# Performance work log

Hardware: AMD Instinct MI355X
Metric: run time of the kernel (lower is better)

The kernel has to match this reference:

```python
import jax, jax.numpy as jnp
import numpy as np

NUM_EXPERTS = 8
K = 2
N_EMBD = 1024
HIDDEN = 4 * N_EMBD
BATCH = 2
SEQ = 1024
LB_SCALE = 0.01
NOISY_STD = 1.0
INIT_S = 0.02


def setup_inputs() -> dict:
    key = jax.random.key(0)
    ks = jax.random.split(key, 8)
    D, H, E = N_EMBD, HIDDEN, NUM_EXPERTS
    return {
        "x": jax.random.normal(ks[0], (BATCH, SEQ, D), jnp.float32),
        "noise": jax.random.normal(ks[1], (BATCH, SEQ, E), jnp.float32),  # torch.randn_like(logits)
        "gate_w": jax.random.normal(ks[2], (E, D), jnp.float32) * INIT_S,
        "noise_weight": jnp.zeros((E,), jnp.float32),  # initialized to zeros in the module
        "w1": jax.random.normal(ks[3], (E, H, D), jnp.float32) * INIT_S,
        "b1": jnp.zeros((E, H), jnp.float32),
        "w2": jax.random.normal(ks[4], (E, H, D), jnp.float32) * INIT_S,
        "b2": jnp.zeros((E, H), jnp.float32),
        "wp": jax.random.normal(ks[5], (E, D, H), jnp.float32) * INIT_S,
        "bp": jnp.zeros((E, D), jnp.float32),
    }


def reference(x, noise, gate_w, noise_weight, w1, b1, w2, b2, wp, bp):
    B, S, D = x.shape
    E = gate_w.shape[0]

    # ---- TopKGateParallel ----
    logits = jnp.einsum('bsd,ed->bse', x, gate_w)           # [B,S,E]
    gate_weights = jax.nn.softmax(logits, axis=-1)
    gw_mean = gate_weights.reshape(-1, E).mean(axis=0)       # [E]
    load_balance_loss = jnp.mean((gw_mean - 1.0 / E) ** 2) * LB_SCALE  # mse vs uniform

    logits_noisy = logits + (noise * NOISY_STD) * noise_weight
    top_v, top_i = jax.lax.top_k(logits_noisy, K)            # [B,S,K]
    # scatter top-k logits into a -inf sea, then softmax -> zeros at non-topk slots
    topk_mask = jnp.sum(jax.nn.one_hot(top_i, E, dtype=jnp.float32), axis=-2) > 0  # [B,S,E]
    sparse_logits = jnp.where(topk_mask, logits_noisy, -jnp.inf)
    top_k_gated_weights = jax.nn.softmax(sparse_logits, axis=-1)  # [B,S,E]

    # ---- expert compute + weighted combine (world_size=1: all experts local) ----
    x_flat = x.reshape(B * S, D)                              # [T,D]
    w_flat = top_k_gated_weights.reshape(B * S, E)            # [T,E]
    y = jnp.zeros_like(x_flat)
    for e in range(E):  # fixed small set of experts
        h = x_flat @ w1[e].T + b1[e]                          # [T,H]
        g = x_flat @ w2[e].T + b2[e]                          # [T,H]
        out_e = (h * jax.nn.silu(g)) @ wp[e].T + bp[e]        # [T,D]
        y = y + w_flat[:, e:e + 1] * out_e
    y = y.reshape(B, S, D)
    return y, load_balance_loss
```

## Files before the change

kernel.cpp:

```cpp
#include <hip/hip_runtime.h>

#define TOK 2048
#define DIM 1024
#define HID 4096
#define NE 8
#define KSPLIT 8
#define TMAX 24

typedef unsigned short u16;
typedef __attribute__((ext_vector_type(8))) short s16x8;
typedef __attribute__((ext_vector_type(4))) float f32x4;

__device__ __forceinline__ u16 f2b(float f) {
  unsigned u = __builtin_bit_cast(unsigned, f);
  unsigned r = (u + 0x7fffu + ((u >> 16) & 1u)) >> 16;
  return (u16)r;
}

__device__ __forceinline__ void gld_lds16(const void* g, void* l) {
  __builtin_amdgcn_global_load_lds((const __attribute__((address_space(1))) void*)g,
                                   (__attribute__((address_space(3))) void*)l, 16, 0, 0);
}

__global__ __launch_bounds__(256) void k_gate(const float* __restrict__ x,
    const float* __restrict__ noise, const float* __restrict__ gw,
    const float* __restrict__ nw,
    int* __restrict__ tok_e, float* __restrict__ tok_w,
    int* __restrict__ bhist, float* __restrict__ bgw, u16* __restrict__ x16) {
  const int wid = threadIdx.x >> 6, lane = threadIdx.x & 63;
  const int t = blockIdx.x * 4 + wid;
  const float* xr = x + (size_t)t * DIM + lane * 16;
  float acc[NE];
#pragma unroll
  for (int e = 0; e < NE; ++e) acc[e] = 0.f;
  u16 xb[16];
#pragma unroll
  for (int j = 0; j < 4; ++j) {
    float4 xv = *(const float4*)(xr + j * 4);
    xb[j * 4 + 0] = f2b(xv.x); xb[j * 4 + 1] = f2b(xv.y);
    xb[j * 4 + 2] = f2b(xv.z); xb[j * 4 + 3] = f2b(xv.w);
#pragma unroll
    for (int e = 0; e < NE; ++e) {
      float4 gv = *(const float4*)(gw + e * DIM + lane * 16 + j * 4);
      acc[e] += xv.x * gv.x + xv.y * gv.y + xv.z * gv.z + xv.w * gv.w;
    }
  }
  *(s16x8*)(x16 + (size_t)t * DIM + lane * 16) = *(const s16x8*)xb;
  *(s16x8*)(x16 + (size_t)t * DIM + lane * 16 + 8) = *(const s16x8*)(xb + 8);
#pragma unroll
  for (int e = 0; e < NE; ++e) {
#pragma unroll
    for (int off = 32; off >= 1; off >>= 1) acc[e] += __shfl_xor(acc[e], off);
  }
  float m = acc[0];
#pragma unroll
  for (int e = 1; e < NE; ++e) m = fmaxf(m, acc[e]);
  float p[NE]; float s = 0.f;
#pragma unroll
  for (int e = 0; e < NE; ++e) { p[e] = expf(acc[e] - m); s += p[e]; }
  float inv = 1.f / s;
  float v[NE];
#pragma unroll
  for (int e = 0; e < NE; ++e) v[e] = acc[e] + noise[t * NE + e] * nw[e];
  float v0 = -3.4e38f, v1 = -3.4e38f; int i0 = 0, i1 = 0;
#pragma unroll
  for (int e = 0; e < NE; ++e) {
    float ve = v[e];
    if (ve > v0) { v1 = v0; i1 = i0; v0 = ve; i0 = e; }
    else if (ve > v1) { v1 = ve; i1 = e; }
  }
  float e1 = expf(v1 - v0);
  float den = 1.f + e1;
  float w0 = 1.f / den, w1v = e1 / den;

  __shared__ float pl[4][NE];
  __shared__ int el[4][2];
  if (lane == 0) {
#pragma unroll
    for (int e = 0; e < NE; ++e) pl[wid][e] = p[e] * inv;
    el[wid][0] = i0; el[wid][1] = i1;
    tok_e[t * 2] = i0; tok_e[t * 2 + 1] = i1;
    tok_w[t * 2] = w0; tok_w[t * 2 + 1] = w1v;
  }
  __syncthreads();
  if (threadIdx.x < NE) {
    const int e = threadIdx.x;
    float ps = pl[0][e] + pl[1][e] + pl[2][e] + pl[3][e];
    int h = 0;
#pragma unroll
    for (int j = 0; j < 4; ++j) {
      h += (el[j][0] == e);
      h += (el[j][1] == e);
    }
    bgw[blockIdx.x * NE + e] = ps;
    bhist[blockIdx.x * NE + e] = h;
  }
}

__global__ __launch_bounds__(512) void k_scan(const int* __restrict__ bhist,
    const float* __restrict__ bgw, int* __restrict__ blk_off, int* __restrict__ prefix,
    int* __restrict__ counts, int* __restrict__ tile_tab, float* __restrict__ loss_out) {
  const int i = threadIdx.x, lane = i & 63, wv = i >> 6;
  __shared__ int wsum[8];
  __shared__ float wfs[8];
  __shared__ int etot[8];
  __shared__ float fsum[8];
  for (int e = 0; e < NE; ++e) {
    int v = bhist[i * NE + e];
    int sc = v;
#pragma unroll
    for (int off = 1; off < 64; off <<= 1) {
      int u = __shfl_up(sc, off);
      if (lane >= off) sc += u;
    }
    float f = bgw[i * NE + e];
#pragma unroll
    for (int off = 32; off >= 1; off >>= 1) f += __shfl_xor(f, off);
    if (lane == 63) wsum[wv] = sc;
    if (lane == 0) wfs[wv] = f;
    __syncthreads();
    int base = 0;
    for (int w2 = 0; w2 < wv; ++w2) base += wsum[w2];
    blk_off[i * NE + e] = base + sc - v;
    if (i == 0) {
      float tf = 0.f;
      for (int w2 = 0; w2 < 8; ++w2) tf += wfs[w2];
      fsum[e] = tf;
    }
    if (i == 511) etot[e] = base + sc;
    __syncthreads();
  }
  if (i == 0) {
    int sacc = 0;
    float l = 0.f;
    int tt = 0;
#pragma unroll
    for (int e = 0; e < NE; ++e) { prefix[e] = sacc; counts[e] = etot[e]; sacc += etot[e]; }
    for (int e = 0; e < NE; ++e) {
      const int nmt = (etot[e] + 255) >> 8;
      for (int m2 = 0; m2 < nmt; ++m2) tile_tab[tt++] = (e << 16) | m2;
    }
    for (; tt < TMAX; ++tt) tile_tab[tt] = -1;
#pragma unroll
    for (int e = 0; e < NE; ++e) {
      float d = fsum[e] * (1.f / TOK) - 0.125f;
      l += d * d;
    }
    *loss_out = l * (0.01f / NE);
  }
}

__global__ __launch_bounds__(256) void k_build(const int* __restrict__ tok_e,
    const float* __restrict__ tok_w, const int* __restrict__ prefix,
    const int* __restrict__ blk_off, int* __restrict__ ent, float* __restrict__ entw,
    int* __restrict__ inv) {
  const int t = blockIdx.x * 256 + threadIdx.x;
  const int g = t >> 2;
  const int base = (t & 3) * 2;
  int ee[8];
#pragma unroll
  for (int j = 0; j < 8; ++j) ee[j] = tok_e[g * 8 + j];
#pragma unroll
  for (int s = 0; s < 2; ++s) {
    const int e = ee[base + s];
    int rank = 0;
#pragma unroll
    for (int j = 0; j < 8; ++j) rank += (j < base + s) && (ee[j] == e);
    const int idx = prefix[e] + blk_off[g * NE + e] + rank;
    ent[idx] = t * 2 + s;
    entw[idx] = tok_w[t * 2 + s];
    inv[t * 2 + s] = idx;
  }
}

__global__ __launch_bounds__(512) void k_gemm1f(const u16* __restrict__ x16,
    const float* __restrict__ w1, const float* __restrict__ w2,
    const float* __restrict__ b1, const float* __restrict__ b2,
    const int* __restrict__ ent, const int* __restrict__ counts,
    const int* __restrict__ prefix, const int* __restrict__ tile_tab,
    u16* __restrict__ act) {
  const int tt = tile_tab[blockIdx.y];
  if (tt < 0) return;
  const int e = tt >> 16, mt = tt & 0xffff, nt = blockIdx.x;
  const int cnt = counts[e];
  const int pfx = prefix[e];
  const int tid = threadIdx.x, w = tid >> 6, l = tid & 63;

  __shared__ u16 smem[2][16384];

  const int r0 = tid >> 2;
  const int c = (tid & 3) ^ ((tid >> 3) & 3);
  int g0 = mt * 256 + r0;       if (g0 >= cnt) g0 = cnt - 1;
  int g1 = mt * 256 + 128 + r0; if (g1 >= cnt) g1 = cnt - 1;
  const u16* sa0 = x16 + (size_t)(ent[pfx + g0] >> 1) * DIM + c * 8;
  const u16* sa1 = x16 + (size_t)(ent[pfx + g1] >> 1) * DIM + c * 8;
  const float* pB1 = w1 + ((size_t)e * HID + nt * 128 + r0) * DIM + c * 8;
  const float* pB2 = w2 + ((size_t)e * HID + nt * 128 + r0) * DIM + c * 8;
  const int oA0 = tid * 8, oA1 = 4096 + tid * 8;
  const int oB1 = 8192 + tid * 8, oB2 = 12288 + tid * 8;

  const int wr = w >> 1, wc = w & 1;
  const int xs = ((l >> 4) ^ ((l >> 1) & 3)) * 8;
  const int ra = (wr * 64 + (l & 15)) * 32 + xs;
  const int rb = (wc * 64 + (l & 15)) * 32 + xs;

  f32x4 acc1[4][4], acc2[4][4];
#pragma unroll
  for (int m = 0; m < 4; ++m)
#pragma unroll
    for (int n = 0; n < 4; ++n) {
      acc1[m][n] = (f32x4){0.f, 0.f, 0.f, 0.f};
      acc2[m][n] = (f32x4){0.f, 0.f, 0.f, 0.f};
    }

  f32x4 a0_, a1_, a2_, a3_;
  f32x4 b0_, b1_, b2_, b3_;

  auto LOADB = [&](f32x4& r0_, f32x4& r1_, f32x4& r2_, f32x4& r3_, int k0) {
    r0_ = *(const f32x4*)(pB1 + k0);
    r1_ = *(const f32x4*)(pB1 + k0 + 4);
    r2_ = *(const f32x4*)(pB2 + k0);
    r3_ = *(const f32x4*)(pB2 + k0 + 4);
  };
  auto STAGEA = [&](int buf, int k0) {
    gld_lds16(sa0 + k0, &smem[buf][oA0]);
    gld_lds16(sa1 + k0, &smem[buf][oA1]);
  };
  auto WRITEB = [&](int buf, const f32x4& r0_, const f32x4& r1_,
                    const f32x4& r2_, const f32x4& r3_) {
    u16 u[16];
    u[0] = f2b(r0_[0]); u[1] = f2b(r0_[1]); u[2] = f2b(r0_[2]); u[3] = f2b(r0_[3]);
    u[4] = f2b(r1_[0]); u[5] = f2b(r1_[1]); u[6] = f2b(r1_[2]); u[7] = f2b(r1_[3]);
    u[8] = f2b(r2_[0]); u[9] = f2b(r2_[1]); u[10] = f2b(r2_[2]); u[11] = f2b(r2_[3]);
    u[12] = f2b(r3_[0]); u[13] = f2b(r3_[1]); u[14] = f2b(r3_[2]); u[15] = f2b(r3_[3]);
    *(s16x8*)&smem[buf][oB1] = *(const s16x8*)u;
    *(s16x8*)&smem[buf][oB2] = *(const s16x8*)(u + 8);
  };
  auto MSTEP = [&](int cur) {
    const u16* S = &smem[cur][0];
    s16x8 af[4];
#pragma unroll
    for (int m = 0; m < 4; ++m) af[m] = *(const s16x8*)(S + ra + m * 512);
    __builtin_amdgcn_s_setprio(1);
#pragma unroll
    for (int n = 0; n < 4; ++n) {
      s16x8 bf1 = *(const s16x8*)(S + 8192 + rb + n * 512);
      s16x8 bf2 = *(const s16x8*)(S + 12288 + rb + n * 512);
#pragma unroll
      for (int m = 0; m < 4; ++m) {
        acc1[m][n] = __builtin_amdgcn_mfma_f32_16x16x32_bf16(af[m], bf1, acc1[m][n], 0, 0, 0);
        acc2[m][n] = __builtin_amdgcn_mfma_f32_16x16x32_bf16(af[m], bf2, acc2[m][n], 0, 0, 0);
      }
    }
    __builtin_amdgcn_s_setprio(0);
  };

  const int NT = DIM / 32;
  LOADB(a0_, a1_, a2_, a3_, 0);
  STAGEA(0, 0);
  LOADB(b0_, b1_, b2_, b3_, 32);
  asm volatile("s_waitcnt vmcnt(4)" ::: "memory");
  __builtin_amdgcn_sched_barrier(0);
  WRITEB(0, a0_, a1_, a2_, a3_);
  STAGEA(1, 32);
  asm volatile("s_waitcnt lgkmcnt(0)" ::: "memory");
  __builtin_amdgcn_sched_barrier(0);
  __builtin_amdgcn_s_barrier();

  for (int kt = 0; kt < NT; kt += 2) {
    if (kt + 2 < NT) LOADB(a0_, a1_, a2_, a3_, (kt + 2) * 32);
    MSTEP(0);
    __builtin_amdgcn_s_barrier();
    if (kt + 2 < NT) asm volatile("s_waitcnt vmcnt(4)" ::: "memory");
    else             asm volatile("s_waitcnt vmcnt(0)" ::: "memory");
    __builtin_amdgcn_sched_barrier(0);
    WRITEB(1, b0_, b1_, b2_, b3_);
    if (kt + 2 < NT) STAGEA(0, (kt + 2) * 32);
    asm volatile("s_waitcnt lgkmcnt(0)" ::: "memory");
    __builtin_amdgcn_sched_barrier(0);
    __builtin_amdgcn_s_barrier();
    if (kt + 3 < NT) LOADB(b0_, b1_, b2_, b3_, (kt + 3) * 32);
    MSTEP(1);
    if (kt + 2 < NT) {
      __builtin_amdgcn_s_barrier();
      if (kt + 3 < NT) asm volatile("s_waitcnt vmcnt(4)" ::: "memory");
      else             asm volatile("s_waitcnt vmcnt(0)" ::: "memory");
      __builtin_amdgcn_sched_barrier(0);
      WRITEB(0, a0_, a1_, a2_, a3_);
      if (kt + 3 < NT) STAGEA(1, (kt + 3) * 32);
      asm volatile("s_waitcnt lgkmcnt(0)" ::: "memory");
      __builtin_amdgcn_sched_barrier(0);
      __builtin_amdgcn_s_barrier();
    }
  }

#pragma unroll
  for (int n = 0; n < 4; ++n) {
    const int col = nt * 128 + wc * 64 + n * 16 + (l & 15);
    const float bb1 = b1[(size_t)e * HID + col];
    const float bb2 = b2[(size_t)e * HID + col];
#pragma unroll
    for (int m = 0; m < 4; ++m) {
#pragma unroll
      for (int r = 0; r < 4; ++r) {
        const int row = mt * 256 + wr * 64 + m * 16 + (l >> 4) * 4 + r;
        if (row < cnt) {
          float h = acc1[m][n][r] + bb1;
          float g = acc2[m][n][r] + bb2;
          float a = h * g / (1.f + expf(-g));
          act[(size_t)(pfx + row) * HID + col] = f2b(a);
        }
      }
    }
  }
}

__global__ __launch_bounds__(512) void k_gemm2f(const u16* __restrict__ act,
    const float* __restrict__ wp, const float* __restrict__ bp,
    const float* __restrict__ entw, const int* __restrict__ counts,
    const int* __restrict__ prefix, const int* __restrict__ tile_tab,
    float* __restrict__ yp) {
  const int tt = tile_tab[blockIdx.y];
  if (tt < 0) return;
  const int e = tt >> 16, mt = tt & 0xffff;
  const int sk = blockIdx.z, nt = blockIdx.x;
  const int cnt = counts[e];
  const int pfx = prefix[e];
  const int tid = threadIdx.x, w = tid >> 6, l = tid & 63;

  __shared__ u16 smem[2][16384];

  const int r0 = tid >> 2;
  const int c = (tid & 3) ^ ((tid >> 3) & 3);
  int g0 = mt * 256 + r0;       if (g0 >= cnt) g0 = cnt - 1;
  int g1 = mt * 256 + 128 + r0; if (g1 >= cnt) g1 = cnt - 1;
  const int kbase = sk * (HID / KSPLIT);
  const u16* sa0 = act + (size_t)(pfx + g0) * HID + kbase + c * 8;
  const u16* sa1 = act + (size_t)(pfx + g1) * HID + kbase + c * 8;
  const float* pB0 = wp + ((size_t)e * DIM + nt * 256 + r0) * HID + kbase + c * 8;
  const float* pB1h = pB0 + (size_t)128 * HID;
  const int oA0 = tid * 8, oA1 = 4096 + tid * 8;
  const int oB0 = 8192 + tid * 8, oB1 = 12288 + tid * 8;

  const int wr = w >> 2, wc = w & 3;
  const int xs = ((l >> 4) ^ ((l >> 1) & 3)) * 8;
  const int ra = (wr * 128 + (l & 15)) * 32 + xs;
  const int rb = 8192 + (wc * 64 + (l & 15)) * 32 + xs;

  f32x4 acc[8][4];
#pragma unroll
  for (int m = 0; m < 8; ++m)
#pragma unroll
    for (int n = 0; n < 4; ++n) acc[m][n] = (f32x4){0.f, 0.f, 0.f, 0.f};

  f32x4 a0_, a1_, a2_, a3_;
  f32x4 b0_, b1_, b2_, b3_;

  auto LOADB = [&](f32x4& r0_, f32x4& r1_, f32x4& r2_, f32x4& r3_, int k0) {
    r0_ = *(const f32x4*)(pB0 + k0);
    r1_ = *(const f32x4*)(pB0 + k0 + 4);
    r2_ = *(const f32x4*)(pB1h + k0);
    r3_ = *(const f32x4*)(pB1h + k0 + 4);
  };
  auto STAGEA = [&](int buf, int k0) {
    gld_lds16(sa0 + k0, &smem[buf][oA0]);
    gld_lds16(sa1 + k0, &smem[buf][oA1]);
  };
  auto WRITEB = [&](int buf, const f32x4& r0_, const f32x4& r1_,
                    const f32x4& r2_, const f32x4& r3_) {
    u16 u[16];
    u[0] = f2b(r0_[0]); u[1] = f2b(r0_[1]); u[2] = f2b(r0_[2]); u[3] = f2b(r0_[3]);
    u[4] = f2b(r1_[0]); u[5] = f2b(r1_[1]); u[6] = f2b(r1_[2]); u[7] = f2b(r1_[3]);
    u[8] = f2b(r2_[0]); u[9] = f2b(r2_[1]); u[10] = f2b(r2_[2]); u[11] = f2b(r2_[3]);
    u[12] = f2b(r3_[0]); u[13] = f2b(r3_[1]); u[14] = f2b(r3_[2]); u[15] = f2b(r3_[3]);
    *(s16x8*)&smem[buf][oB0] = *(const s16x8*)u;
    *(s16x8*)&smem[buf][oB1] = *(const s16x8*)(u + 8);
  };
  auto MSTEP = [&](int cur) {
    const u16* S = &smem[cur][0];
    __builtin_amdgcn_s_setprio(1);
#pragma unroll
    for (int n = 0; n < 4; ++n) {
      s16x8 bf = *(const s16x8*)(S + rb + n * 512);
#pragma unroll
      for (int m = 0; m < 8; ++m) {
        s16x8 af = *(const s16x8*)(S + ra + m * 512);
        acc[m][n] = __builtin_amdgcn_mfma_f32_16x16x32_bf16(af, bf, acc[m][n], 0, 0, 0);
      }
    }
    __builtin_amdgcn_s_setprio(0);
  };

  const int NIT = HID / KSPLIT / 32;
  LOADB(a0_, a1_, a2_, a3_, 0);
  STAGEA(0, 0);
  LOADB(b0_, b1_, b2_, b3_, 32);
  asm volatile("s_waitcnt vmcnt(4)" ::: "memory");
  __builtin_amdgcn_sched_barrier(0);
  WRITEB(0, a0_, a1_, a2_, a3_);
  STAGEA(1, 32);
  asm volatile("s_waitcnt lgkmcnt(0)" ::: "memory");
  __builtin_amdgcn_sched_barrier(0);
  __builtin_amdgcn_s_barrier();

  for (int kt = 0; kt < NIT; kt += 2) {
    if (kt + 2 < NIT) LOADB(a0_, a1_, a2_, a3_, (kt + 2) * 32);
    MSTEP(0);
    __builtin_amdgcn_s_barrier();
    if (kt + 2 < NIT) asm volatile("s_waitcnt vmcnt(4)" ::: "memory");
    else              asm volatile("s_waitcnt vmcnt(0)" ::: "memory");
    __builtin_amdgcn_sched_barrier(0);
    WRITEB(1, b0_, b1_, b2_, b3_);
    if (kt + 2 < NIT) STAGEA(0, (kt + 2) * 32);
    asm volatile("s_waitcnt lgkmcnt(0)" ::: "memory");
    __builtin_amdgcn_sched_barrier(0);
    __builtin_amdgcn_s_barrier();
    if (kt + 3 < NIT) LOADB(b0_, b1_, b2_, b3_, (kt + 3) * 32);
    MSTEP(1);
    if (kt + 2 < NIT) {
      __builtin_amdgcn_s_barrier();
      if (kt + 3 < NIT) asm volatile("s_waitcnt vmcnt(4)" ::: "memory");
      else              asm volatile("s_waitcnt vmcnt(0)" ::: "memory");
      __builtin_amdgcn_sched_barrier(0);
      WRITEB(0, a0_, a1_, a2_, a3_);
      if (kt + 3 < NIT) STAGEA(1, (kt + 3) * 32);
      asm volatile("s_waitcnt lgkmcnt(0)" ::: "memory");
      __builtin_amdgcn_sched_barrier(0);
      __builtin_amdgcn_s_barrier();
    }
  }

#pragma unroll
  for (int n = 0; n < 4; ++n) {
    const int col = nt * 256 + wc * 64 + n * 16 + (l & 15);
    const float bpv = (sk == 0) ? bp[(size_t)e * DIM + col] : 0.f;
#pragma unroll
    for (int m = 0; m < 8; ++m) {
#pragma unroll
      for (int r = 0; r < 4; ++r) {
        const int row = mt * 256 + wr * 128 + m * 16 + (l >> 4) * 4 + r;
        if (row < cnt) {
          const int idx = pfx + row;
          yp[((size_t)sk * (TOK * 2) + idx) * DIM + col] = entw[idx] * (acc[m][n][r] + bpv);
        }
      }
    }
  }
}

__global__ __launch_bounds__(256) void k_final(const float* __restrict__ yp,
    const int* __restrict__ inv, float* __restrict__ out) {
  const int t = blockIdx.x;
  const int d = threadIdx.x * 4;
  const int i0 = inv[t * 2], i1 = inv[t * 2 + 1];
  float4 s = {0.f, 0.f, 0.f, 0.f};
#pragma unroll
  for (int sk = 0; sk < KSPLIT; ++sk) {
    float4 a = *(const float4*)(yp + ((size_t)sk * (TOK * 2) + i0) * DIM + d);
    float4 b = *(const float4*)(yp + ((size_t)sk * (TOK * 2) + i1) * DIM + d);
    s.x += a.x + b.x; s.y += a.y + b.y; s.z += a.z + b.z; s.w += a.w + b.w;
  }
  *(float4*)(out + (size_t)t * DIM + d) = s;
}

extern "C" void kernel_launch(void* const* d_in, const int* in_sizes, int n_in,
                              void* d_out, int out_size, void* d_ws, size_t ws_size,
                              hipStream_t stream) {
  const float* x      = (const float*)d_in[0];
  const float* noise  = (const float*)d_in[1];
  const float* gate_w = (const float*)d_in[2];
  const float* nw     = (const float*)d_in[3];
  const float* w1     = (const float*)d_in[4];
  const float* b1     = (const float*)d_in[5];
  const float* w2     = (const float*)d_in[6];
  const float* b2     = (const float*)d_in[7];
  const float* wp     = (const float*)d_in[8];
  const float* bp     = (const float*)d_in[9];
  float* out = (float*)d_out;
  char* ws = (char*)d_ws;

  const size_t SZ_X16 = (size_t)TOK * DIM * 2;
  const size_t SZ_ACT = (size_t)TOK * 2 * HID * 2;
  const size_t SZ_YP  = (size_t)KSPLIT * TOK * 2 * DIM * 4;

  u16* x16  = (u16*)ws;
  u16* act  = (u16*)(ws + SZ_X16);
  float* yp = (float*)(ws + SZ_X16 + SZ_ACT);
  char* meta = ws + SZ_X16 + SZ_ACT + SZ_YP;
  int*   tok_e    = (int*)(meta);
  float* tok_w    = (float*)(meta + 16384);
  int*   ent      = (int*)(meta + 32768);
  float* entw     = (float*)(meta + 49152);
  int*   bhist    = (int*)(meta + 65536);
  float* bgw      = (float*)(meta + 81920);
  int*   blk_off  = (int*)(meta + 98304);
  int*   inv      = (int*)(meta + 114688);
  int*   counts   = (int*)(meta + 131072);
  int*   prefix   = (int*)(meta + 131072 + 64);
  int*   tile_tab = (int*)(meta + 131072 + 128);

  k_gate<<<TOK / 4, 256, 0, stream>>>(x, noise, gate_w, nw, tok_e, tok_w, bhist, bgw, x16);
  k_scan<<<1, 512, 0, stream>>>(bhist, bgw, blk_off, prefix, counts, tile_tab,
                                out + (size_t)TOK * DIM);
  k_build<<<TOK / 256, 256, 0, stream>>>(tok_e, tok_w, prefix, blk_off, ent, entw, inv);
  k_gemm1f<<<dim3(HID / 128, TMAX), 512, 0, stream>>>(x16, w1, w2, b1, b2, ent,
                                                      counts, prefix, tile_tab, act);
  k_gemm2f<<<dim3(DIM / 256, TMAX, KSPLIT), 512, 0, stream>>>(act, wp, bp, entw,
                                                              counts, prefix, tile_tab, yp);
  k_final<<<TOK, 256, 0, stream>>>(yp, inv, out);
}
```

Baseline: 348.3 us.

## Double K-tile depth to 64 in both expert GEMMs and halve K-split

Both grouped GEMM kernels now stage a 64-wide K slice per pipeline step instead of 32. This doubles the LDS buffers to 64 KB each and re-derives the XOR swizzle for 8 chunks per row. Each step issues two MFMA sub-steps, which halves the number of barriers and waitcnt round trips per K. The second GEMM's split-K factor drops from 8 to 4, reducing partial-sum writes and the reduction traffic at the cost of fewer blocks. The trade-offs are higher register pressure (16 staged f32x4 vectors), larger LDS use that may cap occupancy, and less parallelism in the second GEMM.

```diff
diff --git a/kernel.cpp b/kernel.cpp
--- a/kernel.cpp
+++ b/kernel.cpp
@@ -4,7 +4,7 @@
 #define DIM 1024
 #define HID 4096
 #define NE 8
-#define KSPLIT 8
+#define KSPLIT 4
 #define TMAX 24
 
 typedef unsigned short u16;
@@ -186,23 +186,35 @@
   const int pfx = prefix[e];
   const int tid = threadIdx.x, w = tid >> 6, l = tid & 63;
 
-  __shared__ u16 smem[2][16384];
-
-  const int r0 = tid >> 2;
-  const int c = (tid & 3) ^ ((tid >> 3) & 3);
-  int g0 = mt * 256 + r0;       if (g0 >= cnt) g0 = cnt - 1;
-  int g1 = mt * 256 + 128 + r0; if (g1 >= cnt) g1 = cnt - 1;
-  const u16* sa0 = x16 + (size_t)(ent[pfx + g0] >> 1) * DIM + c * 8;
-  const u16* sa1 = x16 + (size_t)(ent[pfx + g1] >> 1) * DIM + c * 8;
-  const float* pB1 = w1 + ((size_t)e * HID + nt * 128 + r0) * DIM + c * 8;
-  const float* pB2 = w2 + ((size_t)e * HID + nt * 128 + r0) * DIM + c * 8;
-  const int oA0 = tid * 8, oA1 = 4096 + tid * 8;
-  const int oB1 = 8192 + tid * 8, oB2 = 12288 + tid * 8;
+  __shared__ u16 smem[2][32768];
+
+  const int gcA = (tid & 7) ^ ((tid >> 3) & 7);
+  const u16* srcA[4];
+  int dstA[4];
+#pragma unroll
+  for (int q = 0; q < 4; ++q) {
+    const int rr = q * 64 + (tid >> 3);
+    int g = mt * 256 + rr; if (g >= cnt) g = cnt - 1;
+    srcA[q] = x16 + (size_t)(ent[pfx + g] >> 1) * DIM + gcA * 8;
+    dstA[q] = rr * 64 + (tid & 7) * 8;
+  }
+  const int rB = tid >> 2;
+  const float* pB1 = w1 + ((size_t)e * HID + nt * 128 + rB) * DIM + (tid & 3) * 16;
+  const float* pB2 = w2 + ((size_t)e * HID + nt * 128 + rB) * DIM + (tid & 3) * 16;
+  const int s0 = ((tid & 3) * 2) ^ (rB & 7);
+  const int s1 = s0 ^ 1;
+  const int wbB1 = 16384 + rB * 64;
+  const int wbB2 = 24576 + rB * 64;
 
   const int wr = w >> 1, wc = w & 1;
-  const int xs = ((l >> 4) ^ ((l >> 1) & 3)) * 8;
-  const int ra = (wr * 64 + (l & 15)) * 32 + xs;
-  const int rb = (wc * 64 + (l & 15)) * 32 + xs;
+  const int rowA = wr * 64 + (l & 15);
+  const int aBase = rowA * 64;
+  const int aX0 = (((l >> 4)) ^ (rowA & 7)) * 8;
+  const int aX1 = ((4 | (l >> 4)) ^ (rowA & 7)) * 8;
+  const int rowB = wc * 64 + (l & 15);
+  const int bBase = rowB * 64;
+  const int bX0 = (((l >> 4)) ^ (rowB & 7)) * 8;
+  const int bX1 = ((4 | (l >> 4)) ^ (rowB & 7)) * 8;
 
   f32x4 acc1[4][4], acc2[4][4];
 #pragma unroll
@@ -213,81 +225,91 @@
       acc2[m][n] = (f32x4){0.f, 0.f, 0.f, 0.f};
     }
 
-  f32x4 a0_, a1_, a2_, a3_;
-  f32x4 b0_, b1_, b2_, b3_;
-
-  auto LOADB = [&](f32x4& r0_, f32x4& r1_, f32x4& r2_, f32x4& r3_, int k0) {
-    r0_ = *(const f32x4*)(pB1 + k0);
-    r1_ = *(const f32x4*)(pB1 + k0 + 4);
-    r2_ = *(const f32x4*)(pB2 + k0);
-    r3_ = *(const f32x4*)(pB2 + k0 + 4);
-  };
-  auto STAGEA = [&](int buf, int k0) {
-    gld_lds16(sa0 + k0, &smem[buf][oA0]);
-    gld_lds16(sa1 + k0, &smem[buf][oA1]);
-  };
-  auto WRITEB = [&](int buf, const f32x4& r0_, const f32x4& r1_,
-                    const f32x4& r2_, const f32x4& r3_) {
-    u16 u[16];
-    u[0] = f2b(r0_[0]); u[1] = f2b(r0_[1]); u[2] = f2b(r0_[2]); u[3] = f2b(r0_[3]);
-    u[4] = f2b(r1_[0]); u[5] = f2b(r1_[1]); u[6] = f2b(r1_[2]); u[7] = f2b(r1_[3]);
-    u[8] = f2b(r2_[0]); u[9] = f2b(r2_[1]); u[10] = f2b(r2_[2]); u[11] = f2b(r2_[3]);
-    u[12] = f2b(r3_[0]); u[13] = f2b(r3_[1]); u[14] = f2b(r3_[2]); u[15] = f2b(r3_[3]);
-    *(s16x8*)&smem[buf][oB1] = *(const s16x8*)u;
-    *(s16x8*)&smem[buf][oB2] = *(const s16x8*)(u + 8);
-  };
-  auto MSTEP = [&](int cur) {
-    const u16* S = &smem[cur][0];
-    s16x8 af[4];
-#pragma unroll
-    for (int m = 0; m < 4; ++m) af[m] = *(const s16x8*)(S + ra + m * 512);
-    __builtin_amdgcn_s_setprio(1);
-#pragma unroll
-    for (int n = 0; n < 4; ++n) {
-      s16x8 bf1 = *(const s16x8*)(S + 8192 + rb + n * 512);
-      s16x8 bf2 = *(const s16x8*)(S + 12288 + rb + n * 512);
-#pragma unroll
-      for (int m = 0; m < 4; ++m) {
-        acc1[m][n] = __builtin_amdgcn_mfma_f32_16x16x32_bf16(af[m], bf1, acc1[m][n], 0, 0, 0);
-        acc2[m][n] = __builtin_amdgcn_mfma_f32_16x16x32_bf16(af[m], bf2, acc2[m][n], 0, 0, 0);
+  f32x4 rgA[8], rgB[8];
+
+  auto LOADB = [&](f32x4 (&r)[8], int kt) {
+    const float* p1 = pB1 + kt * 64;
+    const float* p2 = pB2 + kt * 64;
+#pragma unroll
+    for (int j = 0; j < 4; ++j) {
+      r[j] = *(const f32x4*)(p1 + j * 4);
+      r[4 + j] = *(const f32x4*)(p2 + j * 4);
+    }
+  };
+  auto STAGEA = [&](int buf, int kt) {
+#pragma unroll
+    for (int q = 0; q < 4; ++q) gld_lds16(srcA[q] + kt * 64, &smem[buf][dstA[q]]);
+  };
+  auto WRITEB = [&](int buf, const f32x4 (&r)[8]) {
+    u16 u[32];
+#pragma unroll
+    for (int j = 0; j < 4; ++j) {
+      u[j * 4 + 0] = f2b(r[j][0]); u[j * 4 + 1] = f2b(r[j][1]);
+      u[j * 4 + 2] = f2b(r[j][2]); u[j * 4 + 3] = f2b(r[j][3]);
+      u[16 + j * 4 + 0] = f2b(r[4 + j][0]); u[16 + j * 4 + 1] = f2b(r[4 + j][1]);
+      u[16 + j * 4 + 2] = f2b(r[4 + j][2]); u[16 + j * 4 + 3] = f2b(r[4 + j][3]);
+    }
+    *(s16x8*)&smem[buf][wbB1 + s0 * 8] = *(const s16x8*)u;
+    *(s16x8*)&smem[buf][wbB1 + s1 * 8] = *(const s16x8*)(u + 8);
+    *(s16x8*)&smem[buf][wbB2 + s0 * 8] = *(const s16x8*)(u + 16);
+    *(s16x8*)&smem[buf][wbB2 + s1 * 8] = *(const s16x8*)(u + 24);
+  };
+  auto MSTEP = [&](int buf) {
+#pragma unroll
+    for (int kk = 0; kk < 2; ++kk) {
+      const int aX = kk ? aX1 : aX0;
+      const int bX = kk ? bX1 : bX0;
+      s16x8 af[4];
+#pragma unroll
+      for (int m = 0; m < 4; ++m) af[m] = *(const s16x8*)&smem[buf][aBase + m * 1024 + aX];
+      __builtin_amdgcn_s_setprio(1);
+#pragma unroll
+      for (int n = 0; n < 4; ++n) {
+        s16x8 bf1 = *(const s16x8*)&smem[buf][16384 + bBase + n * 1024 + bX];
+        s16x8 bf2 = *(const s16x8*)&smem[buf][24576 + bBase + n * 1024 + bX];
+#pragma unroll
+        for (int m = 0; m < 4; ++m) {
+          acc1[m][n] = __builtin_amdgcn_mfma_f32_16x16x32_bf16(af[m], bf1, acc1[m][n], 0, 0, 0);
+          acc2[m][n] = __builtin_amdgcn_mfma_f32_16x16x32_bf16(af[m], bf2, acc2[m][n], 0, 0, 0);
+        }
       }
-    }
-    __builtin_amdgcn_s_setprio(0);
-  };
-
-  const int NT = DIM / 32;
-  LOADB(a0_, a1_, a2_, a3_, 0);
+      __builtin_amdgcn_s_setprio(0);
+    }
+  };
+
+  const int NT = DIM / 64;
+  LOADB(rgA, 0);
   STAGEA(0, 0);
-  LOADB(b0_, b1_, b2_, b3_, 32);
-  asm volatile("s_waitcnt vmcnt(4)" ::: "memory");
+  LOADB(rgB, 1);
+  asm volatile("s_waitcnt vmcnt(8)" ::: "memory");
   __builtin_amdgcn_sched_barrier(0);
-  WRITEB(0, a0_, a1_, a2_, a3_);
-  STAGEA(1, 32);
+  WRITEB(0, rgA);
+  STAGEA(1, 1);
   asm volatile("s_waitcnt lgkmcnt(0)" ::: "memory");
   __builtin_amdgcn_sched_barrier(0);
   __builtin_amdgcn_s_barrier();
 
   for (int kt = 0; kt < NT; kt += 2) {
-    if (kt + 2 < NT) LOADB(a0_, a1_, a2_, a3_, (kt + 2) * 32);
+    if (kt + 2 < NT) LOADB(rgA, kt + 2);
     MSTEP(0);
     __builtin_amdgcn_s_barrier();
-    if (kt + 2 < NT) asm volatile("s_waitcnt vmcnt(4)" ::: "memory");
+    if (kt + 2 < NT) asm volatile("s_waitcnt vmcnt(8)" ::: "memory");
     else             asm volatile("s_waitcnt vmcnt(0)" ::: "memory");
     __builtin_amdgcn_sched_barrier(0);
-    WRITEB(1, b0_, b1_, b2_, b3_);
-    if (kt + 2 < NT) STAGEA(0, (kt + 2) * 32);
+    WRITEB(1, rgB);
+    if (kt + 2 < NT) STAGEA(0, kt + 2);
     asm volatile("s_waitcnt lgkmcnt(0)" ::: "memory");
     __builtin_amdgcn_sched_barrier(0);
     __builtin_amdgcn_s_barrier();
-    if (kt + 3 < NT) LOADB(b0_, b1_, b2_, b3_, (kt + 3) * 32);
+    if (kt + 3 < NT) LOADB(rgB, kt + 3);
     MSTEP(1);
     if (kt + 2 < NT) {
       __builtin_amdgcn_s_barrier();
-      if (kt + 3 < NT) asm volatile("s_waitcnt vmcnt(4)" ::: "memory");
+      if (kt + 3 < NT) asm volatile("s_waitcnt vmcnt(8)" ::: "memory");
       else             asm volatile("s_waitcnt vmcnt(0)" ::: "memory");
       __builtin_amdgcn_sched_barrier(0);
-      WRITEB(0, a0_, a1_, a2_, a3_);
-      if (kt + 3 < NT) STAGEA(1, (kt + 3) * 32);
+      WRITEB(0, rgA);
+      if (kt + 3 < NT) STAGEA(1, kt + 3);
       asm volatile("s_waitcnt lgkmcnt(0)" ::: "memory");
       __builtin_amdgcn_sched_barrier(0);
       __builtin_amdgcn_s_barrier();
@@ -328,24 +350,33 @@
   const int pfx = prefix[e];
   const int tid = threadIdx.x, w = tid >> 6, l = tid & 63;
 
-  __shared__ u16 smem[2][16384];
-
-  const int r0 = tid >> 2;
-  const int c = (tid & 3) ^ ((tid >> 3) & 3);
-  int g0 = mt * 256 + r0;       if (g0 >= cnt) g0 = cnt - 1;
-  int g1 = mt * 256 + 128 + r0; if (g1 >= cnt) g1 = cnt - 1;
+  __shared__ u16 smem[2][32768];
+
   const int kbase = sk * (HID / KSPLIT);
-  const u16* sa0 = act + (size_t)(pfx + g0) * HID + kbase + c * 8;
-  const u16* sa1 = act + (size_t)(pfx + g1) * HID + kbase + c * 8;
-  const float* pB0 = wp + ((size_t)e * DIM + nt * 256 + r0) * HID + kbase + c * 8;
-  const float* pB1h = pB0 + (size_t)128 * HID;
-  const int oA0 = tid * 8, oA1 = 4096 + tid * 8;
-  const int oB0 = 8192 + tid * 8, oB1 = 12288 + tid * 8;
+  const int gcA = (tid & 7) ^ ((tid >> 3) & 7);
+  const u16* srcA[4];
+  int dstA[4];
+#pragma unroll
+  for (int q = 0; q < 4; ++q) {
+    const int rr = q * 64 + (tid >> 3);
+    int g = mt * 256 + rr; if (g >= cnt) g = cnt - 1;
+    srcA[q] = act + (size_t)(pfx + g) * HID + kbase + gcA * 8;
+    dstA[q] = rr * 64 + (tid & 7) * 8;
+  }
+  const int rB = tid >> 1;
+  const float* pB = wp + ((size_t)e * DIM + nt * 256 + rB) * HID + kbase + (tid & 1) * 32;
+  const int xwB = rB & 7;
+  const int wbB = 16384 + rB * 64;
 
   const int wr = w >> 2, wc = w & 3;
-  const int xs = ((l >> 4) ^ ((l >> 1) & 3)) * 8;
-  const int ra = (wr * 128 + (l & 15)) * 32 + xs;
-  const int rb = 8192 + (wc * 64 + (l & 15)) * 32 + xs;
+  const int rowA = wr * 128 + (l & 15);
+  const int aBase = rowA * 64;
+  const int aX0 = (((l >> 4)) ^ (rowA & 7)) * 8;
+  const int aX1 = ((4 | (l >> 4)) ^ (rowA & 7)) * 8;
+  const int rowB = wc * 64 + (l & 15);
+  const int bBase = rowB * 64;
+  const int bX0 = (((l >> 4)) ^ (rowB & 7)) * 8;
+  const int bX1 = ((4 | (l >> 4)) ^ (rowB & 7)) * 8;
 
   f32x4 acc[8][4];
 #pragma unroll
@@ -353,77 +384,83 @@
 #pragma unroll
     for (int n = 0; n < 4; ++n) acc[m][n] = (f32x4){0.f, 0.f, 0.f, 0.f};
 
-  f32x4 a0_, a1_, a2_, a3_;
-  f32x4 b0_, b1_, b2_, b3_;
-
-  auto LOADB = [&](f32x4& r0_, f32x4& r1_, f32x4& r2_, f32x4& r3_, int k0) {
-    r0_ = *(const f32x4*)(pB0 + k0);
-    r1_ = *(const f32x4*)(pB0 + k0 + 4);
-    r2_ = *(const f32x4*)(pB1h + k0);
-    r3_ = *(const f32x4*)(pB1h + k0 + 4);
-  };
-  auto STAGEA = [&](int buf, int k0) {
-    gld_lds16(sa0 + k0, &smem[buf][oA0]);
-    gld_lds16(sa1 + k0, &smem[buf][oA1]);
-  };
-  auto WRITEB = [&](int buf, const f32x4& r0_, const f32x4& r1_,
-                    const f32x4& r2_, const f32x4& r3_) {
-    u16 u[16];
-    u[0] = f2b(r0_[0]); u[1] = f2b(r0_[1]); u[2] = f2b(r0_[2]); u[3] = f2b(r0_[3]);
-    u[4] = f2b(r1_[0]); u[5] = f2b(r1_[1]); u[6] = f2b(r1_[2]); u[7] = f2b(r1_[3]);
-    u[8] = f2b(r2_[0]); u[9] = f2b(r2_[1]); u[10] = f2b(r2_[2]); u[11] = f2b(r2_[3]);
-    u[12] = f2b(r3_[0]); u[13] = f2b(r3_[1]); u[14] = f2b(r3_[2]); u[15] = f2b(r3_[3]);
-    *(s16x8*)&smem[buf][oB0] = *(const s16x8*)u;
-    *(s16x8*)&smem[buf][oB1] = *(const s16x8*)(u + 8);
-  };
-  auto MSTEP = [&](int cur) {
-    const u16* S = &smem[cur][0];
-    __builtin_amdgcn_s_setprio(1);
-#pragma unroll
-    for (int n = 0; n < 4; ++n) {
-      s16x8 bf = *(const s16x8*)(S + rb + n * 512);
+  f32x4 rgA[8], rgB[8];
+
+  auto LOADB = [&](f32x4 (&r)[8], int kt) {
+    const float* p = pB + kt * 64;
+#pragma unroll
+    for (int j = 0; j < 8; ++j) r[j] = *(const f32x4*)(p + j * 4);
+  };
+  auto STAGEA = [&](int buf, int kt) {
+#pragma unroll
+    for (int q = 0; q < 4; ++q) gld_lds16(srcA[q] + kt * 64, &smem[buf][dstA[q]]);
+  };
+  auto WRITEB = [&](int buf, const f32x4 (&r)[8]) {
+    u16 u[32];
+#pragma unroll
+    for (int j = 0; j < 8; ++j) {
+      u[j * 4 + 0] = f2b(r[j][0]); u[j * 4 + 1] = f2b(r[j][1]);
+      u[j * 4 + 2] = f2b(r[j][2]); u[j * 4 + 3] = f2b(r[j][3]);
+    }
+#pragma unroll
+    for (int j2 = 0; j2 < 4; ++j2) {
+      const int ch = (tid & 1) * 4 + j2;
+      *(s16x8*)&smem[buf][wbB + ((ch ^ xwB) * 8)] = *(const s16x8*)(u + j2 * 8);
+    }
+  };
+  auto MSTEP = [&](int buf) {
+#pragma unroll
+    for (int kk = 0; kk < 2; ++kk) {
+      const int aX = kk ? aX1 : aX0;
+      const int bX = kk ? bX1 : bX0;
+      s16x8 bf[4];
+#pragma unroll
+      for (int n = 0; n < 4; ++n) bf[n] = *(const s16x8*)&smem[buf][16384 + bBase + n * 1024 + bX];
+      __builtin_amdgcn_s_setprio(1);
 #pragma unroll
       for (int m = 0; m < 8; ++m) {
-        s16x8 af = *(const s16x8*)(S + ra + m * 512);
-        acc[m][n] = __builtin_amdgcn_mfma_f32_16x16x32_bf16(af, bf, acc[m][n], 0, 0, 0);
+        s16x8 af = *(const s16x8*)&smem[buf][aBase + m * 1024 + aX];
+#pragma unroll
+        for (int n = 0; n < 4; ++n)
+          acc[m][n] = __builtin_amdgcn_mfma_f32_16x16x32_bf16(af, bf[n], acc[m][n], 0, 0, 0);
       }
-    }
-    __builtin_amdgcn_s_setprio(0);
-  };
-
-  const int NIT = HID / KSPLIT / 32;
-  LOADB(a0_, a1_, a2_, a3_, 0);
+      __builtin_amdgcn_s_setprio(0);
+    }
+  };
+
+  const int NT = HID / KSPLIT / 64;
+  LOADB(rgA, 0);
   STAGEA(0, 0);
-  LOADB(b0_, b1_, b2_, b3_, 32);
-  asm volatile("s_waitcnt vmcnt(4)" ::: "memory");
+  LOADB(rgB, 1);
+  asm volatile("s_waitcnt vmcnt(8)" ::: "memory");
   __builtin_amdgcn_sched_barrier(0);
-  WRITEB(0, a0_, a1_, a2_, a3_);
-  STAGEA(1, 32);
+  WRITEB(0, rgA);
+  STAGEA(1, 1);
   asm volatile("s_waitcnt lgkmcnt(0)" ::: "memory");
   __builtin_amdgcn_sched_barrier(0);
   __builtin_amdgcn_s_barrier();
 
-  for (int kt = 0; kt < NIT; kt += 2) {
-    if (kt + 2 < NIT) LOADB(a0_, a1_, a2_, a3_, (kt + 2) * 32);
+  for (int kt = 0; kt < NT; kt += 2) {
+    if (kt + 2 < NT) LOADB(rgA, kt + 2);
     MSTEP(0);
     __builtin_amdgcn_s_barrier();
-    if (kt + 2 < NIT) asm volatile("s_waitcnt vmcnt(4)" ::: "memory");
-    else              asm volatile("s_waitcnt vmcnt(0)" ::: "memory");
+    if (kt + 2 < NT) asm volatile("s_waitcnt vmcnt(8)" ::: "memory");
+    else             asm volatile("s_waitcnt vmcnt(0)" ::: "memory");
     __builtin_amdgcn_sched_barrier(0);
-    WRITEB(1, b0_, b1_, b2_, b3_);
-    if (kt + 2 < NIT) STAGEA(0, (kt + 2) * 32);
+    WRITEB(1, rgB);
+    if (kt + 2 < NT) STAGEA(0, kt + 2);
     asm volatile("s_waitcnt lgkmcnt(0)" ::: "memory");
     __builtin_amdgcn_sched_barrier(0);
     __builtin_amdgcn_s_barrier();
-    if (kt + 3 < NIT) LOADB(b0_, b1_, b2_, b3_, (kt + 3) * 32);
+    if (kt + 3 < NT) LOADB(rgB, kt + 3);
     MSTEP(1);
-    if (kt + 2 < NIT) {
+    if (kt + 2 < NT) {
       __builtin_amdgcn_s_barrier();
-      if (kt + 3 < NIT) asm volatile("s_waitcnt vmcnt(4)" ::: "memory");
-      else              asm volatile("s_waitcnt vmcnt(0)" ::: "memory");
+      if (kt + 3 < NT) asm volatile("s_waitcnt vmcnt(8)" ::: "memory");
+      else             asm volatile("s_waitcnt vmcnt(0)" ::: "memory");
       __builtin_amdgcn_sched_barrier(0);
-      WRITEB(0, a0_, a1_, a2_, a3_);
-      if (kt + 3 < NIT) STAGEA(1, (kt + 3) * 32);
+      WRITEB(0, rgA);
+      if (kt + 3 < NT) STAGEA(1, kt + 3);
       asm volatile("s_waitcnt lgkmcnt(0)" ::: "memory");
       __builtin_amdgcn_sched_barrier(0);
       __builtin_amdgcn_s_barrier();
```

Measured after the change: 752.9 us. 2.16x slower.
